# Optimization experiments

Measured on AMD Instinct MI355X. Metric: run time of the kernel, lower is better.

The kernel has to match this reference:

```python
import jax, jax.numpy as jnp
import numpy as np
from jax import lax

N_HEADS = 8
D_KEYS = 128
HALF = D_KEYS // 2
N_KEYS = 256          # sub-keys per set; n_experts = N_KEYS**2
TOP_K = 8
D_MODEL = 512


def setup_inputs() -> dict:
    key = jax.random.key(0)
    ks = jax.random.split(key, 6)
    N, T = 2, 1024
    queries = jax.random.normal(ks[0], (N, T, D_MODEL), dtype=jnp.float32)
    Wq = jax.random.normal(ks[1], (D_MODEL, N_HEADS * D_KEYS), dtype=jnp.float32) / np.sqrt(D_MODEL)
    bq = jnp.zeros((N_HEADS * D_KEYS,), dtype=jnp.float32)
    bound = 1.0 / np.sqrt(HALF)
    keys = jax.random.uniform(ks[2], (N_HEADS, 2, N_KEYS, HALF), dtype=jnp.float32,
                              minval=-bound, maxval=bound)
    w_down = jax.random.normal(ks[3], (N_KEYS * N_KEYS, D_MODEL), dtype=jnp.float32) * 0.02
    w_up = jax.random.normal(ks[4], (N_KEYS * N_KEYS, D_MODEL), dtype=jnp.float32) * 0.02
    return {"queries": queries, "Wq": Wq, "bq": bq, "keys": keys,
            "w_down": w_down, "w_up": w_up}


def _forward(queries, Wq, bq, keys, w_down, w_up):
    N, T, D = queries.shape
    x = queries.reshape(-1, D)                                   # [B, D], B = N*T
    q = (x @ Wq + bq).reshape(-1, N_HEADS, D_KEYS)               # [B, H, d_keys]

    # product-key routing: score each half-query against each sub-key set
    q1, q2 = q[..., :HALF], q[..., HALF:]
    s1 = jnp.einsum('bhc,hnc->bhn', q1, keys[:, 0])              # [B, H, n_keys]
    s2 = jnp.einsum('bhc,hnc->bhn', q2, keys[:, 1])
    s1t, i1 = lax.top_k(s1, TOP_K)                               # [B, H, k]
    s2t, i2 = lax.top_k(s2, TOP_K)

    # cartesian product of the two top-k sets, then re-top-k
    all_scores = (s1t[..., :, None] + s2t[..., None, :]).reshape(-1, N_HEADS, TOP_K * TOP_K)
    all_idx = (i1[..., :, None] * N_KEYS + i2[..., None, :]).reshape(-1, N_HEADS, TOP_K * TOP_K)
    scores, best = lax.top_k(all_scores, TOP_K)                  # [B, H, k]
    indices = jnp.take_along_axis(all_idx, best, axis=-1)        # [B, H, k]

    # gather per-token expert weights and combine (PEER single-neuron experts)
    w_d = w_down[indices]                                        # [B, H, k, D]
    w_u = w_up[indices]                                          # [B, H, k, D]
    inner = jnp.einsum('bd,bhkd->bhk', x, w_d)                   # [B, H, k]
    vals = jax.nn.relu(inner) * jax.nn.softmax(scores, axis=-1)
    out = jnp.einsum('bhk,bhkd->bd', vals, w_u)                  # [B, D]
    return out.reshape(N, T, D)


def reference(queries, Wq, bq, keys, w_down, w_up):
    return _forward(queries, Wq, bq, keys, w_down, w_up)
```

## Files before the change

### kernel.cpp

```cpp
#include <hip/hip_runtime.h>
#include <math.h>

#define D_MODEL 512
#define NH      8
#define DK      128
#define HALFD   64
#define NKEYS   256
#define TOPK    8
#define NTOK    2048

__global__ __launch_bounds__(256) void qproj_gemm(const float* __restrict__ A,
                                                  const float* __restrict__ B,
                                                  const float* __restrict__ bias,
                                                  float* __restrict__ C) {
  const int N = NH * DK, K = D_MODEL;
  __shared__ float As[16][68];
  __shared__ float Bs[16][68];
  int tid = threadIdx.x;
  int tx = tid & 15, ty = tid >> 4;
  int m0 = blockIdx.y * 64, n0 = blockIdx.x * 64;
  int arow = tid >> 2, akk = (tid & 3) << 2;
  int bkr = tid >> 4, bnn = (tid & 15) << 2;
  const float* Aptr = A + (size_t)(m0 + arow) * K + akk;
  const float* Bptr = B + (size_t)bkr * N + n0 + bnn;

  float4 aReg = *(const float4*)Aptr;
  float4 bReg = *(const float4*)Bptr;

  float c[4][4];
#pragma unroll
  for (int i = 0; i < 4; ++i)
#pragma unroll
    for (int j = 0; j < 4; ++j) c[i][j] = 0.f;

  for (int k0 = 0; k0 < K; k0 += 16) {
    As[akk + 0][arow] = aReg.x;
    As[akk + 1][arow] = aReg.y;
    As[akk + 2][arow] = aReg.z;
    As[akk + 3][arow] = aReg.w;
    *(float4*)&Bs[bkr][bnn] = bReg;
    __syncthreads();
    if (k0 + 16 < K) {
      aReg = *(const float4*)(Aptr + k0 + 16);
      bReg = *(const float4*)(Bptr + (size_t)(k0 + 16) * N);
    }
#pragma unroll
    for (int k = 0; k < 16; ++k) {
      float4 a = *(const float4*)&As[k][ty << 2];
      float4 b = *(const float4*)&Bs[k][tx << 2];
      float av[4] = {a.x, a.y, a.z, a.w};
      float bv[4] = {b.x, b.y, b.z, b.w};
#pragma unroll
      for (int i = 0; i < 4; ++i)
#pragma unroll
        for (int j = 0; j < 4; ++j) c[i][j] += av[i] * bv[j];
    }
    __syncthreads();
  }
#pragma unroll
  for (int i = 0; i < 4; ++i) {
    int m = m0 + (ty << 2) + i;
#pragma unroll
    for (int j = 0; j < 4; ++j) {
      int n = n0 + (tx << 2) + j;
      C[(size_t)m * N + n] = c[i][j] + bias[n];
    }
  }
}

__global__ __launch_bounds__(256) void score_gemm(const float* __restrict__ qbuf,
                                                  const float* __restrict__ keys,
                                                  float* __restrict__ scores) {
  __shared__ float As[16][68];
  __shared__ float Bs[16][68];
  int tid = threadIdx.x;
  int tx = tid & 15, ty = tid >> 4;
  int n0 = blockIdx.x * 64, m0 = blockIdx.y * 64, slab = blockIdx.z;
  const float* Ap = qbuf + (size_t)slab * HALFD;
  const float* Bp = keys + (size_t)slab * NKEYS * HALFD;
  float c[4][4];
#pragma unroll
  for (int i = 0; i < 4; ++i)
#pragma unroll
    for (int j = 0; j < 4; ++j) c[i][j] = 0.f;

  for (int k0 = 0; k0 < HALFD; k0 += 16) {
    int row = tid >> 2, kk = (tid & 3) << 2;
    {
      float4 av = *(const float4*)(Ap + (size_t)(m0 + row) * (NH * DK) + k0 + kk);
      As[kk + 0][row] = av.x;
      As[kk + 1][row] = av.y;
      As[kk + 2][row] = av.z;
      As[kk + 3][row] = av.w;
    }
    {
      float4 bv = *(const float4*)(Bp + (size_t)(n0 + row) * HALFD + k0 + kk);
      Bs[kk + 0][row] = bv.x;
      Bs[kk + 1][row] = bv.y;
      Bs[kk + 2][row] = bv.z;
      Bs[kk + 3][row] = bv.w;
    }
    __syncthreads();
#pragma unroll
    for (int k = 0; k < 16; ++k) {
      float4 a = *(const float4*)&As[k][ty << 2];
      float4 b = *(const float4*)&Bs[k][tx << 2];
      float av[4] = {a.x, a.y, a.z, a.w};
      float bv[4] = {b.x, b.y, b.z, b.w};
#pragma unroll
      for (int i = 0; i < 4; ++i)
#pragma unroll
        for (int j = 0; j < 4; ++j) c[i][j] += av[i] * bv[j];
    }
    __syncthreads();
  }
#pragma unroll
  for (int i = 0; i < 4; ++i) {
    int m = m0 + (ty << 2) + i;
    float4 cv = make_float4(c[i][0], c[i][1], c[i][2], c[i][3]);
    *(float4*)&scores[((size_t)m * 16 + slab) * NKEYS + n0 + (tx << 2)] = cv;
  }
}

#define CE(a, b)                                                        \
  do {                                                                  \
    if (lv[a] < lv[b] || (lv[a] == lv[b] && li[a] > li[b])) {           \
      float tv_ = lv[a]; lv[a] = lv[b]; lv[b] = tv_;                    \
      int ti_ = li[a]; li[a] = li[b]; li[b] = ti_;                      \
    }                                                                   \
  } while (0)

__global__ __launch_bounds__(256) void topk_kernel(const float* __restrict__ scores,
                                                   int* __restrict__ widx,
                                                   float* __restrict__ wval) {
  int tid = threadIdx.x;
  int task = blockIdx.x * 4 + (tid >> 6);
  int ln = tid & 63;
  int b = task >> 3, h = task & 7;
  int s = ln >> 5, l = ln & 31;

  const float* sp = scores + ((size_t)b * 16 + h * 2 + s) * NKEYS + l * 8;
  float lv[8];
  int li[8];
  {
    float4 v0 = *(const float4*)sp;
    float4 v1 = *(const float4*)(sp + 4);
    lv[0] = v0.x; lv[1] = v0.y; lv[2] = v0.z; lv[3] = v0.w;
    lv[4] = v1.x; lv[5] = v1.y; lv[6] = v1.z; lv[7] = v1.w;
#pragma unroll
    for (int m = 0; m < 8; ++m) li[m] = l * 8 + m;
  }
  CE(0, 1); CE(2, 3); CE(0, 2); CE(1, 3); CE(1, 2);
  CE(4, 5); CE(6, 7); CE(4, 6); CE(5, 7); CE(5, 6);
  CE(0, 4); CE(1, 5); CE(2, 6); CE(3, 7);
  CE(2, 4); CE(3, 5);
  CE(1, 2); CE(3, 4); CE(5, 6);

  float wv_cap = 0.f;
  int wn_cap = 0;
#pragma unroll
  for (int k = 0; k < 8; ++k) {
    float v = lv[0];
    int n = li[0];
#pragma unroll
    for (int off = 16; off; off >>= 1) {
      float ov = __shfl_xor(v, off);
      int on = __shfl_xor(n, off);
      if (ov > v || (ov == v && on < n)) { v = ov; n = on; }
    }
    if (l == k) { wv_cap = v; wn_cap = n; }
    if (li[0] == n) {
#pragma unroll
      for (int m = 0; m < 7; ++m) { lv[m] = lv[m + 1]; li[m] = li[m + 1]; }
      lv[7] = -INFINITY;
      li[7] = 1 << 30;
    }
  }

  int i = ln >> 3, j = ln & 7;
  float v_i = __shfl(wv_cap, i);
  float v_j = __shfl(wv_cap, 32 + j);
  int n_i = __shfl(wn_cap, i);
  int n_j = __shfl(wn_cap, 32 + j);
  float cv = v_i + v_j;
  int ci = n_i * NKEYS + n_j;
  int p = ln;
#pragma unroll
  for (int k = 2; k <= 64; k <<= 1) {
#pragma unroll
    for (int j2 = k >> 1; j2 > 0; j2 >>= 1) {
      float ov = __shfl_xor(cv, j2);
      int op = __shfl_xor(p, j2);
      bool descBlock = ((ln & k) == 0);
      bool lower = ((ln & j2) == 0);
      bool mineBefore = (cv > ov) || (cv == ov && p < op);
      bool keep = (descBlock == lower) ? mineBefore : !mineBefore;
      if (!keep) { cv = ov; p = op; }
    }
  }
  float m0 = __shfl(cv, 0);
  float e = expf(cv - m0);
  float d = e;
#pragma unroll
  for (int off = 1; off < 8; off <<= 1) d += __shfl_xor(d, off);
  int wci = __shfl(ci, p);
  if (ln < TOPK) {
    size_t o = ((size_t)b * NH + h) * TOPK + ln;
    wval[o] = e / d;
    widx[o] = wci;
  }
}

__global__ __launch_bounds__(1024) void gather_fused(const float* __restrict__ x,
                                                     const float* __restrict__ w_down,
                                                     const float* __restrict__ w_up,
                                                     const int* __restrict__ widx,
                                                     const float* __restrict__ wval,
                                                     float* __restrict__ out) {
  int b = blockIdx.x;
  int tid = threadIdx.x;
  int ln = tid & 63, w = tid >> 6;
  __shared__ float part[16][D_MODEL];
  __shared__ float vals_lds[64];
  __shared__ int   idx_lds[64];
  __shared__ float cval[64];
  __shared__ int   cidx[64];
  __shared__ int   nlive_sh;

  int pbase = b * 64 + w * 4;
  const float4* xr = (const float4*)(x + (size_t)b * D_MODEL);
  float4 x0 = xr[ln * 2], x1 = xr[ln * 2 + 1];

  int idx0 = widx[pbase + 0];
  int idx1 = widx[pbase + 1];
  int idx2 = widx[pbase + 2];
  int idx3 = widx[pbase + 3];
  const float4* r0 = (const float4*)(w_down + (size_t)idx0 * D_MODEL);
  const float4* r1 = (const float4*)(w_down + (size_t)idx1 * D_MODEL);
  const float4* r2 = (const float4*)(w_down + (size_t)idx2 * D_MODEL);
  const float4* r3 = (const float4*)(w_down + (size_t)idx3 * D_MODEL);
  float4 a0 = r0[ln * 2], b0 = r0[ln * 2 + 1];
  float4 a1 = r1[ln * 2], b1 = r1[ln * 2 + 1];
  float4 a2 = r2[ln * 2], b2 = r2[ln * 2 + 1];
  float4 a3 = r3[ln * 2], b3 = r3[ln * 2 + 1];

  float d0 = x0.x * a0.x + x0.y * a0.y + x0.z * a0.z + x0.w * a0.w +
             x1.x * b0.x + x1.y * b0.y + x1.z * b0.z + x1.w * b0.w;
  float d1 = x0.x * a1.x + x0.y * a1.y + x0.z * a1.z + x0.w * a1.w +
             x1.x * b1.x + x1.y * b1.y + x1.z * b1.z + x1.w * b1.w;
  float d2 = x0.x * a2.x + x0.y * a2.y + x0.z * a2.z + x0.w * a2.w +
             x1.x * b2.x + x1.y * b2.y + x1.z * b2.z + x1.w * b2.w;
  float d3 = x0.x * a3.x + x0.y * a3.y + x0.z * a3.z + x0.w * a3.w +
             x1.x * b3.x + x1.y * b3.y + x1.z * b3.z + x1.w * b3.w;

#pragma unroll
  for (int off = 32; off; off >>= 1) {
    d0 += __shfl_xor(d0, off);
    d1 += __shfl_xor(d1, off);
    d2 += __shfl_xor(d2, off);
    d3 += __shfl_xor(d3, off);
  }
  if (ln == 0) {
    vals_lds[w * 4 + 0] = fmaxf(d0, 0.f) * wval[pbase + 0];
    vals_lds[w * 4 + 1] = fmaxf(d1, 0.f) * wval[pbase + 1];
    vals_lds[w * 4 + 2] = fmaxf(d2, 0.f) * wval[pbase + 2];
    vals_lds[w * 4 + 3] = fmaxf(d3, 0.f) * wval[pbase + 3];
    idx_lds[w * 4 + 0] = idx0;
    idx_lds[w * 4 + 1] = idx1;
    idx_lds[w * 4 + 2] = idx2;
    idx_lds[w * 4 + 3] = idx3;
  }
  __syncthreads();

  if (w == 0) {
    float v = vals_lds[ln];
    int id = idx_lds[ln];
    bool live = v > 0.f;
    unsigned long long mask = __ballot(live);
    int pos = __popcll(mask & ((1ull << ln) - 1ull));
    if (live) { cval[pos] = v; cidx[pos] = id; }
    if (ln == 0) nlive_sh = (int)__popcll(mask);
  }
  __syncthreads();
  int nlive = nlive_sh;

  float4 ua[4], ub[4];
  float vv[4];
  bool act[4];
#pragma unroll
  for (int r = 0; r < 4; ++r) {
    int p = w + r * 16;
    act[r] = (p < nlive);
    if (act[r]) {
      vv[r] = cval[p];
      const float4* wu = (const float4*)(w_up + (size_t)cidx[p] * D_MODEL);
      ua[r] = wu[ln * 2];
      ub[r] = wu[ln * 2 + 1];
    }
  }
  float oa[8];
#pragma unroll
  for (int e = 0; e < 8; ++e) oa[e] = 0.f;
#pragma unroll
  for (int r = 0; r < 4; ++r) {
    if (act[r]) {
      float v = vv[r];
      oa[0] += v * ua[r].x; oa[1] += v * ua[r].y; oa[2] += v * ua[r].z; oa[3] += v * ua[r].w;
      oa[4] += v * ub[r].x; oa[5] += v * ub[r].y; oa[6] += v * ub[r].z; oa[7] += v * ub[r].w;
    }
  }

  *(float4*)&part[w][ln * 8]     = make_float4(oa[0], oa[1], oa[2], oa[3]);
  *(float4*)&part[w][ln * 8 + 4] = make_float4(oa[4], oa[5], oa[6], oa[7]);
  __syncthreads();
  if (tid < D_MODEL) {
    float acc = 0.f;
#pragma unroll
    for (int ww = 0; ww < 16; ++ww) acc += part[ww][tid];
    out[(size_t)b * D_MODEL + tid] = acc;
  }
}

extern "C" void kernel_launch(void* const* d_in, const int* in_sizes, int n_in,
                              void* d_out, int out_size, void* d_ws, size_t ws_size,
                              hipStream_t stream) {
  const float* queries = (const float*)d_in[0];
  const float* Wq      = (const float*)d_in[1];
  const float* bq      = (const float*)d_in[2];
  const float* keys    = (const float*)d_in[3];
  const float* w_down  = (const float*)d_in[4];
  const float* w_up    = (const float*)d_in[5];
  float* outp = (float*)d_out;

  char* base = (char*)d_ws;
  float* qbuf   = (float*)base;
  float* scores = (float*)(base + (size_t)8 * 1024 * 1024);
  int*   widx   = (int*)(base + (size_t)42 * 1024 * 1024);
  float* wval   = (float*)(base + (size_t)43 * 1024 * 1024);

  qproj_gemm<<<dim3(16, 32), 256, 0, stream>>>(queries, Wq, bq, qbuf);
  score_gemm<<<dim3(4, 32, 16), 256, 0, stream>>>(qbuf, keys, scores);
  topk_kernel<<<4096, 256, 0, stream>>>(scores, widx, wval);
  gather_fused<<<2048, 1024, 0, stream>>>(queries, w_down, w_up, widx, wval, outp);
}
```

Measured before the change: 145.4 us.

## Double-buffer qproj GEMM tiles and split expert gather into two half-token blocks

```diff
diff --git a/kernel.cpp b/kernel.cpp
--- a/kernel.cpp
+++ b/kernel.cpp
@@ -14,8 +14,8 @@
                                                   const float* __restrict__ bias,
                                                   float* __restrict__ C) {
   const int N = NH * DK, K = D_MODEL;
-  __shared__ float As[16][68];
-  __shared__ float Bs[16][68];
+  __shared__ float As[2][16][68];
+  __shared__ float Bs[2][16][68];
   int tid = threadIdx.x;
   int tx = tid & 15, ty = tid >> 4;
   int m0 = blockIdx.y * 64, n0 = blockIdx.x * 64;
@@ -26,6 +26,12 @@
 
   float4 aReg = *(const float4*)Aptr;
   float4 bReg = *(const float4*)Bptr;
+  As[0][akk + 0][arow] = aReg.x;
+  As[0][akk + 1][arow] = aReg.y;
+  As[0][akk + 2][arow] = aReg.z;
+  As[0][akk + 3][arow] = aReg.w;
+  *(float4*)&Bs[0][bkr][bnn] = bReg;
+  __syncthreads();
 
   float c[4][4];
 #pragma unroll
@@ -33,27 +39,30 @@
 #pragma unroll
     for (int j = 0; j < 4; ++j) c[i][j] = 0.f;
 
-  for (int k0 = 0; k0 < K; k0 += 16) {
-    As[akk + 0][arow] = aReg.x;
-    As[akk + 1][arow] = aReg.y;
-    As[akk + 2][arow] = aReg.z;
-    As[akk + 3][arow] = aReg.w;
-    *(float4*)&Bs[bkr][bnn] = bReg;
-    __syncthreads();
-    if (k0 + 16 < K) {
-      aReg = *(const float4*)(Aptr + k0 + 16);
-      bReg = *(const float4*)(Bptr + (size_t)(k0 + 16) * N);
+  for (int it = 0; it < 32; ++it) {
+    int cur = it & 1;
+    if (it + 1 < 32) {
+      aReg = *(const float4*)(Aptr + (it + 1) * 16);
+      bReg = *(const float4*)(Bptr + (size_t)(it + 1) * 16 * N);
     }
 #pragma unroll
     for (int k = 0; k < 16; ++k) {
-      float4 a = *(const float4*)&As[k][ty << 2];
-      float4 b = *(const float4*)&Bs[k][tx << 2];
+      float4 a = *(const float4*)&As[cur][k][ty << 2];
+      float4 b = *(const float4*)&Bs[cur][k][tx << 2];
       float av[4] = {a.x, a.y, a.z, a.w};
       float bv[4] = {b.x, b.y, b.z, b.w};
 #pragma unroll
       for (int i = 0; i < 4; ++i)
 #pragma unroll
         for (int j = 0; j < 4; ++j) c[i][j] += av[i] * bv[j];
+    }
+    if (it + 1 < 32) {
+      int nxt = cur ^ 1;
+      As[nxt][akk + 0][arow] = aReg.x;
+      As[nxt][akk + 1][arow] = aReg.y;
+      As[nxt][akk + 2][arow] = aReg.z;
+      As[nxt][akk + 3][arow] = aReg.w;
+      *(float4*)&Bs[nxt][bkr][bnn] = bReg;
     }
     __syncthreads();
   }
@@ -211,23 +220,24 @@
   }
 }
 
-__global__ __launch_bounds__(1024) void gather_fused(const float* __restrict__ x,
-                                                     const float* __restrict__ w_down,
-                                                     const float* __restrict__ w_up,
-                                                     const int* __restrict__ widx,
-                                                     const float* __restrict__ wval,
-                                                     float* __restrict__ out) {
-  int b = blockIdx.x;
+__global__ __launch_bounds__(512) void gather_half(const float* __restrict__ x,
+                                                   const float* __restrict__ w_down,
+                                                   const float* __restrict__ w_up,
+                                                   const int* __restrict__ widx,
+                                                   const float* __restrict__ wval,
+                                                   float* __restrict__ partial) {
+  int blk = blockIdx.x;
+  int b = blk >> 1, half = blk & 1;
   int tid = threadIdx.x;
   int ln = tid & 63, w = tid >> 6;
-  __shared__ float part[16][D_MODEL];
-  __shared__ float vals_lds[64];
-  __shared__ int   idx_lds[64];
-  __shared__ float cval[64];
-  __shared__ int   cidx[64];
+  __shared__ float part[8][D_MODEL];
+  __shared__ float vals_lds[32];
+  __shared__ int   idx_lds[32];
+  __shared__ float cval[32];
+  __shared__ int   cidx[32];
   __shared__ int   nlive_sh;
 
-  int pbase = b * 64 + w * 4;
+  int pbase = b * 64 + half * 32 + w * 4;
   const float4* xr = (const float4*)(x + (size_t)b * D_MODEL);
   float4 x0 = xr[ln * 2], x1 = xr[ln * 2 + 1];
 
@@ -273,9 +283,10 @@
   __syncthreads();
 
   if (w == 0) {
-    float v = vals_lds[ln];
-    int id = idx_lds[ln];
-    bool live = v > 0.f;
+    bool inr = ln < 32;
+    float v = inr ? vals_lds[ln] : 0.f;
+    int id = inr ? idx_lds[ln] : 0;
+    bool live = inr && (v > 0.f);
     unsigned long long mask = __ballot(live);
     int pos = __popcll(mask & ((1ull << ln) - 1ull));
     if (live) { cval[pos] = v; cidx[pos] = id; }
@@ -289,7 +300,7 @@
   bool act[4];
 #pragma unroll
   for (int r = 0; r < 4; ++r) {
-    int p = w + r * 16;
+    int p = w + r * 8;
     act[r] = (p < nlive);
     if (act[r]) {
       vv[r] = cval[p];
@@ -313,12 +324,20 @@
   *(float4*)&part[w][ln * 8]     = make_float4(oa[0], oa[1], oa[2], oa[3]);
   *(float4*)&part[w][ln * 8 + 4] = make_float4(oa[4], oa[5], oa[6], oa[7]);
   __syncthreads();
-  if (tid < D_MODEL) {
-    float acc = 0.f;
-#pragma unroll
-    for (int ww = 0; ww < 16; ++ww) acc += part[ww][tid];
-    out[(size_t)b * D_MODEL + tid] = acc;
-  }
+  {
+    int d = tid;
+    float acc = part[0][d] + part[1][d] + part[2][d] + part[3][d] +
+                part[4][d] + part[5][d] + part[6][d] + part[7][d];
+    partial[(size_t)blk * D_MODEL + d] = acc;
+  }
+}
+
+__global__ __launch_bounds__(512) void merge_out(const float* __restrict__ partial,
+                                                 float* __restrict__ out) {
+  int b = blockIdx.x;
+  int d = threadIdx.x;
+  out[(size_t)b * D_MODEL + d] =
+      partial[(size_t)(b * 2) * D_MODEL + d] + partial[(size_t)(b * 2 + 1) * D_MODEL + d];
 }
 
 extern "C" void kernel_launch(void* const* d_in, const int* in_sizes, int n_in,
@@ -333,13 +352,15 @@
   float* outp = (float*)d_out;
 
   char* base = (char*)d_ws;
-  float* qbuf   = (float*)base;
-  float* scores = (float*)(base + (size_t)8 * 1024 * 1024);
-  int*   widx   = (int*)(base + (size_t)42 * 1024 * 1024);
-  float* wval   = (float*)(base + (size_t)43 * 1024 * 1024);
+  float* qbuf    = (float*)base;
+  float* scores  = (float*)(base + (size_t)8 * 1024 * 1024);
+  int*   widx    = (int*)(base + (size_t)42 * 1024 * 1024);
+  float* wval    = (float*)(base + (size_t)43 * 1024 * 1024);
+  float* partial = (float*)base;
 
   qproj_gemm<<<dim3(16, 32), 256, 0, stream>>>(queries, Wq, bq, qbuf);
   score_gemm<<<dim3(4, 32, 16), 256, 0, stream>>>(qbuf, keys, scores);
   topk_kernel<<<4096, 256, 0, stream>>>(scores, widx, wval);
-  gather_fused<<<2048, 1024, 0, stream>>>(queries, w_down, w_up, widx, wval, outp);
-}
+  gather_half<<<4096, 512, 0, stream>>>(queries, w_down, w_up, widx, wval, partial);
+  merge_out<<<2048, 512, 0, stream>>>(partial, outp);
+}
```

Result: slower. 152.1 us (+4.6%).
